# Kernel optimization log

Measured on AMD Instinct MI355X. Metric: run time of the kernel, lower is better.

## Reference

```python
import jax, jax.numpy as jnp
import numpy as np

B, C, H, W, R = 8, 3, 1024, 1024, 32
SMOOTH = 1e-5
SRPI = float(np.sqrt(2.0 * np.pi))
S_K = float(2.0 ** (1.0 / 1e11))  # s ** (1/k) with s=2, k=1e11 -> ~1.0
NORM = 2.50635


def setup_inputs() -> dict:
    key = jax.random.key(0)
    k1, k2, k3, k4, k5, k6 = jax.random.split(key, 6)
    x = jax.random.normal(k1, (B, C + 1, H, W), dtype=jnp.float32)
    y = jax.random.randint(k2, (B, 1, H, W), 0, C).astype(jnp.int32)
    cent_i = jax.random.randint(k3, (B, R), 0, H).astype(jnp.int32)
    cent_j = jax.random.randint(k4, (B, R), 0, W).astype(jnp.int32)
    # bbox = (min_row, min_col, max_row, max_col), exclusive ends, min < max
    rows = jnp.sort(jax.random.randint(k5, (B, R, 2), 0, H), axis=-1)
    cols = jnp.sort(jax.random.randint(k6, (B, R, 2), 0, W), axis=-1)
    bbox = jnp.stack([rows[..., 0], cols[..., 0], rows[..., 1] + 1, cols[..., 1] + 1], axis=-1).astype(jnp.int32)
    return dict(x=x, y=y, cent_i=cent_i, cent_j=cent_j, bbox=bbox)


def _density_map(cent_i, cent_j, bbox):
    # sharpen(): sum over ALL region centroids of a unit-width gaussian,
    # evaluated only on pixels inside the union of region bboxes, / 2.50635.
    ii = jnp.arange(H, dtype=jnp.float32)
    jj = jnp.arange(W, dtype=jnp.float32)
    inv2s2 = 1.0 / (2.0 * S_K ** 2)
    gi = jnp.exp(-((ii[None, None, :] - cent_i[:, :, None].astype(jnp.float32)) ** 2) * inv2s2)  # [B,R,H]
    gj = jnp.exp(-((jj[None, None, :] - cent_j[:, :, None].astype(jnp.float32)) ** 2) * inv2s2)  # [B,R,W]
    field = (1.0 / (SRPI * S_K)) * jnp.einsum('brh,brw->bhw', gi, gj)  # separable gaussian sum
    io = jnp.arange(H, dtype=bbox.dtype)
    jo = jnp.arange(W, dtype=bbox.dtype)
    rowin = ((io[None, None, :] >= bbox[:, :, 0:1]) & (io[None, None, :] < bbox[:, :, 2:3])).astype(jnp.float32)  # [B,R,H]
    colin = ((jo[None, None, :] >= bbox[:, :, 1:2]) & (jo[None, None, :] < bbox[:, :, 3:4])).astype(jnp.float32)  # [B,R,W]
    inside = jnp.einsum('brh,brw->bhw', rowin, colin) > 0  # union of bboxes
    return jnp.where(inside, field, 0.0)[:, None] / NORM  # [B,1,H,W]


def _loss(x, y, dm):
    # SoftDiceLoss(softmax_helper, batch_dice=False, smooth=1e-5, do_bg=False)
    probs = jax.nn.softmax(x[:, :C], axis=1)  # [B,C,H,W]
    onehot = (y == jnp.arange(C, dtype=y.dtype)[None, :, None, None]).astype(probs.dtype)
    tp = jnp.sum(probs * onehot, axis=(2, 3))          # [B,C]
    fp = jnp.sum(probs * (1.0 - onehot), axis=(2, 3))
    fn = jnp.sum((1.0 - probs) * onehot, axis=(2, 3))
    dc = (2.0 * tp + SMOOTH) / (2.0 * tp + fp + fn + SMOOTH)
    dice_loss = -jnp.mean(dc[:, 1:])  # do_bg=False drops channel 0
    # RobustCrossEntropyLoss(x[:, -1:], dm): target = dm[:,0].long(); single-channel CE
    lsm = jax.nn.log_softmax(x[:, C:C + 1], axis=1)  # [B,1,H,W] (== 0 for 1 channel)
    tgt = jnp.clip(dm.astype(jnp.int32), 0, 0)       # .long() truncation; valid class range is {0}
    ce = -jnp.mean(jnp.take_along_axis(lsm, tgt, axis=1))
    return dice_loss + ce


def reference(x, y, cent_i, cent_j, bbox):
    dm = _density_map(cent_i, cent_j, bbox)
    return _loss(x, y, dm)
```

## Files before the change

### kernel.cpp

```cpp
#include <hip/hip_runtime.h>

constexpr int B_ = 8;
constexpr int HW = 1024 * 1024;
constexpr int Q = HW / 4;
constexpr int BLOCKS_X = 256;
constexpr int THREADS = 256;
constexpr int STRIDE = BLOCKS_X * THREADS;
constexpr int ITERS = Q / STRIDE;
constexpr float SMOOTH = 1e-5f;


__global__ __launch_bounds__(256) void dice_stats_kernel(
    const float* __restrict__ x,
    const int* __restrict__ y,
    float* __restrict__ ws)
{
    const int b = blockIdx.y;
    const float* xb = x + (size_t)b * 4 * HW;
    const int*   yb = y + (size_t)b * HW;

    const int base = blockIdx.x * THREADS + threadIdx.x;

    float tp1 = 0.f, tp2 = 0.f, sp1 = 0.f, sp2 = 0.f;
    int   c1 = 0, c2 = 0;

#pragma unroll
    for (int it = 0; it < ITERS; ++it) {
        const int i = base + it * STRIDE;

        float4 a0 = ((const float4*)(xb))[i];
        float4 a1 = ((const float4*)(xb + HW))[i];
        float4 a2 = ((const float4*)(xb + 2 * HW))[i];
        int4   yv = ((const int4*)(yb))[i];

        float v0[4] = {a0.x, a0.y, a0.z, a0.w};
        float v1[4] = {a1.x, a1.y, a1.z, a1.w};
        float v2[4] = {a2.x, a2.y, a2.z, a2.w};
        int   yy[4] = {yv.x, yv.y, yv.z, yv.w};

#pragma unroll
        for (int j = 0; j < 4; ++j) {
            float e0 = __expf(v0[j]);
            float e1 = __expf(v1[j]);
            float e2 = __expf(v2[j]);
            float inv = __builtin_amdgcn_rcpf(e0 + e1 + e2);
            float p1 = e1 * inv;
            float p2 = e2 * inv;
            sp1 += p1;
            sp2 += p2;
            if (yy[j] == 1) { tp1 += p1; c1 += 1; }
            else if (yy[j] == 2) { tp2 += p2; c2 += 1; }
        }
    }

    float fc1 = (float)c1, fc2 = (float)c2;

#pragma unroll
    for (int off = 32; off > 0; off >>= 1) {
        tp1 += __shfl_down(tp1, off);
        tp2 += __shfl_down(tp2, off);
        sp1 += __shfl_down(sp1, off);
        sp2 += __shfl_down(sp2, off);
        fc1 += __shfl_down(fc1, off);
        fc2 += __shfl_down(fc2, off);
    }

    __shared__ float red[4][6];
    const int lane = threadIdx.x & 63;
    const int wave = threadIdx.x >> 6;
    if (lane == 0) {
        red[wave][0] = tp1; red[wave][1] = tp2;
        red[wave][2] = sp1; red[wave][3] = sp2;
        red[wave][4] = fc1; red[wave][5] = fc2;
    }
    __syncthreads();
    if (threadIdx.x < 6) {
        float s = red[0][threadIdx.x] + red[1][threadIdx.x] + red[2][threadIdx.x] + red[3][threadIdx.x];
        ws[((size_t)b * BLOCKS_X + blockIdx.x) * 6 + threadIdx.x] = s;
    }
}

__global__ __launch_bounds__(256) void dice_finalize_kernel(
    const float* __restrict__ ws, float* __restrict__ out)
{
    __shared__ float red[256][6];
    __shared__ float bs[8];
    const int t = threadIdx.x;
    const int b = t >> 5;
    const int l = t & 31;

    float s[6] = {0.f, 0.f, 0.f, 0.f, 0.f, 0.f};
    for (int e = l; e < BLOCKS_X; e += 32) {
        const float* w = ws + ((size_t)b * BLOCKS_X + e) * 6;
#pragma unroll
        for (int k = 0; k < 6; ++k) s[k] += w[k];
    }
#pragma unroll
    for (int k = 0; k < 6; ++k) red[t][k] = s[k];
    __syncthreads();

    if (l == 0) {
        float a[6] = {0.f, 0.f, 0.f, 0.f, 0.f, 0.f};
        for (int e = 0; e < 32; ++e)
#pragma unroll
            for (int k = 0; k < 6; ++k) a[k] += red[b * 32 + e][k];
        float dc1 = (2.0f * a[0] + SMOOTH) / (a[2] + a[4] + SMOOTH);
        float dc2 = (2.0f * a[1] + SMOOTH) / (a[3] + a[5] + SMOOTH);
        bs[b] = dc1 + dc2;
    }
    __syncthreads();
    if (t == 0) {
        float acc = 0.f;
#pragma unroll
        for (int bb = 0; bb < 8; ++bb) acc += bs[bb];
        out[0] = -acc * (1.0f / 16.0f);
    }
}

extern "C" void kernel_launch(void* const* d_in, const int* in_sizes, int n_in,
                              void* d_out, int out_size, void* d_ws, size_t ws_size,
                              hipStream_t stream) {
    const float* x = (const float*)d_in[0];
    const int*   y = (const int*)d_in[1];

    float* ws  = (float*)d_ws;
    float* out = (float*)d_out;

    dim3 grid(BLOCKS_X, B_);
    dice_stats_kernel<<<grid, THREADS, 0, stream>>>(x, y, ws);
    dice_finalize_kernel<<<1, 256, 0, stream>>>(ws, out);
}
```

Measured before the change: 31.70 us.

## Double grid blocks, hoist loads upfront, use shifted softmax and packed counters

Doubles the number of blocks per batch so each thread handles two float4 groups, and issues all eight vector loads before any compute to increase memory-level parallelism. Softmax is rewritten relative to channel 0, which drops one exp per pixel. Branches become selects, and the two label counts are packed into one int so the wave reduction needs one fewer shuffle. The hardcoded two-iteration body relies on ITERS being 2, and with 64 lanes × 8 pixels each count per wave stays far below 2^16. The finalize kernel now reads twice as many partials.

```diff
diff --git a/kernel.cpp b/kernel.cpp
--- a/kernel.cpp
+++ b/kernel.cpp
@@ -3,7 +3,7 @@
 constexpr int B_ = 8;
 constexpr int HW = 1024 * 1024;
 constexpr int Q = HW / 4;
-constexpr int BLOCKS_X = 256;
+constexpr int BLOCKS_X = 512;
 constexpr int THREADS = 256;
 constexpr int STRIDE = BLOCKS_X * THREADS;
 constexpr int ITERS = Q / STRIDE;
@@ -19,41 +19,43 @@
     const float* xb = x + (size_t)b * 4 * HW;
     const int*   yb = y + (size_t)b * HW;
 
-    const int base = blockIdx.x * THREADS + threadIdx.x;
+    const int i0 = blockIdx.x * THREADS + threadIdx.x;
+    const int i1 = i0 + STRIDE;
+
+    float4 a0x = ((const float4*)(xb))[i0];
+    float4 a1x = ((const float4*)(xb + HW))[i0];
+    float4 a2x = ((const float4*)(xb + 2 * HW))[i0];
+    int4   yvx = ((const int4*)(yb))[i0];
+    float4 a0y = ((const float4*)(xb))[i1];
+    float4 a1y = ((const float4*)(xb + HW))[i1];
+    float4 a2y = ((const float4*)(xb + 2 * HW))[i1];
+    int4   yvy = ((const int4*)(yb))[i1];
 
     float tp1 = 0.f, tp2 = 0.f, sp1 = 0.f, sp2 = 0.f;
     int   c1 = 0, c2 = 0;
 
-#pragma unroll
-    for (int it = 0; it < ITERS; ++it) {
-        const int i = base + it * STRIDE;
-
-        float4 a0 = ((const float4*)(xb))[i];
-        float4 a1 = ((const float4*)(xb + HW))[i];
-        float4 a2 = ((const float4*)(xb + 2 * HW))[i];
-        int4   yv = ((const int4*)(yb))[i];
-
-        float v0[4] = {a0.x, a0.y, a0.z, a0.w};
-        float v1[4] = {a1.x, a1.y, a1.z, a1.w};
-        float v2[4] = {a2.x, a2.y, a2.z, a2.w};
-        int   yy[4] = {yv.x, yv.y, yv.z, yv.w};
+    float v0[8] = {a0x.x, a0x.y, a0x.z, a0x.w, a0y.x, a0y.y, a0y.z, a0y.w};
+    float v1[8] = {a1x.x, a1x.y, a1x.z, a1x.w, a1y.x, a1y.y, a1y.z, a1y.w};
+    float v2[8] = {a2x.x, a2x.y, a2x.z, a2x.w, a2y.x, a2y.y, a2y.z, a2y.w};
+    int   yy[8] = {yvx.x, yvx.y, yvx.z, yvx.w, yvy.x, yvy.y, yvy.z, yvy.w};
 
 #pragma unroll
-        for (int j = 0; j < 4; ++j) {
-            float e0 = __expf(v0[j]);
-            float e1 = __expf(v1[j]);
-            float e2 = __expf(v2[j]);
-            float inv = __builtin_amdgcn_rcpf(e0 + e1 + e2);
-            float p1 = e1 * inv;
-            float p2 = e2 * inv;
-            sp1 += p1;
-            sp2 += p2;
-            if (yy[j] == 1) { tp1 += p1; c1 += 1; }
-            else if (yy[j] == 2) { tp2 += p2; c2 += 1; }
-        }
+    for (int j = 0; j < 8; ++j) {
+        float E1 = __expf(v1[j] - v0[j]);
+        float E2 = __expf(v2[j] - v0[j]);
+        float inv = __builtin_amdgcn_rcpf(1.0f + E1 + E2);
+        float p1 = E1 * inv;
+        float p2 = E2 * inv;
+        sp1 += p1;
+        sp2 += p2;
+        bool is1 = (yy[j] == 1), is2 = (yy[j] == 2);
+        tp1 += is1 ? p1 : 0.0f;
+        tp2 += is2 ? p2 : 0.0f;
+        c1 += is1 ? 1 : 0;
+        c2 += is2 ? 1 : 0;
     }
 
-    float fc1 = (float)c1, fc2 = (float)c2;
+    int cc = c1 | (c2 << 16);
 
 #pragma unroll
     for (int off = 32; off > 0; off >>= 1) {
@@ -61,8 +63,7 @@
         tp2 += __shfl_down(tp2, off);
         sp1 += __shfl_down(sp1, off);
         sp2 += __shfl_down(sp2, off);
-        fc1 += __shfl_down(fc1, off);
-        fc2 += __shfl_down(fc2, off);
+        cc  += __shfl_down(cc, off);
     }
 
     __shared__ float red[4][6];
@@ -71,7 +72,8 @@
     if (lane == 0) {
         red[wave][0] = tp1; red[wave][1] = tp2;
         red[wave][2] = sp1; red[wave][3] = sp2;
-        red[wave][4] = fc1; red[wave][5] = fc2;
+        red[wave][4] = (float)(cc & 0xFFFF);
+        red[wave][5] = (float)(cc >> 16);
     }
     __syncthreads();
     if (threadIdx.x < 6) {
```

After: 33.95 us. 7.1% more time.
